# Kernel optimization log

Hardware: AMD Instinct MI355X
Metric: run time of the kernel (lower is better)

## Reference

```python
import jax, jax.numpy as jnp
import numpy as np

B, T, C = 4, 2048, 1024
H = 16
D = C // H  # head_dim = 64
SCALE = D ** -0.5


def setup_inputs() -> dict:
    key = jax.random.key(0)
    k1, k2, k3 = jax.random.split(key, 3)
    x = jax.random.normal(k1, (B, T, C), dtype=jnp.float32)
    w_qkv = jax.random.normal(k2, (C, 3 * C), dtype=jnp.float32) * (C ** -0.5)
    w_proj = jax.random.normal(k3, (C, C), dtype=jnp.float32) * (C ** -0.5)
    return {"x": x, "w_qkv": w_qkv, "w_proj": w_proj}


def reference(x, w_qkv, w_proj):
    Bx, Tx, Cx = x.shape
    qkv = x @ w_qkv                        # [B, T, 3C]
    q, k, v = jnp.split(qkv, 3, axis=-1)   # each [B, T, C]
    # [B, T, H, D] -> [B, H, T, D]
    q = q.reshape(Bx, Tx, H, D).transpose(0, 2, 1, 3)
    k = k.reshape(Bx, Tx, H, D).transpose(0, 2, 1, 3)
    v = v.reshape(Bx, Tx, H, D).transpose(0, 2, 1, 3)
    att = jnp.einsum('bhqd,bhkd->bhqk', q, k) * SCALE  # [B, H, T, T]
    causal = jnp.tril(jnp.ones((Tx, Tx), dtype=bool))
    att = jnp.where(causal[None, None], att, -jnp.inf)
    att = jax.nn.softmax(att, axis=-1)
    # dropout p=0.0 (eval-mode reference): identity
    y = jnp.einsum('bhqk,bhkd->bhqd', att, v)          # [B, H, T, D]
    y = y.transpose(0, 2, 1, 3).reshape(Bx, Tx, Cx)    # [B, T, C]
    return y @ w_proj
```

## Files before the change

kernel.cpp:

```cpp
#include <hip/hip_runtime.h>
#include <hip/hip_bf16.h>

#define Bdim 4
#define Tdim 2048
#define Cdim 1024
#define Hdim 16
#define Ddim 64
#define SCALE_Q 0.18033688011112042f

using f32x4  = __attribute__((ext_vector_type(4))) float;
using short8 = __attribute__((ext_vector_type(8))) short;

union U8 { uint4 v; unsigned short s[8]; };

__device__ __forceinline__ unsigned short f2bf(float f) {
  union { float f; unsigned int i; } x; x.f = f;
  unsigned int lsb = (x.i >> 16) & 1u;
  unsigned int r = x.i + 0x7fffu + lsb;
  return (unsigned short)(r >> 16);
}

__device__ __forceinline__ unsigned int pk_bf16(float lo, float hi) {
  union { __hip_bfloat162 h; unsigned int u; } c;
  c.h = __float22bfloat162_rn(make_float2(lo, hi));
  return c.u;
}

__device__ __forceinline__ float fexp2(float x) {
#if __has_builtin(__builtin_amdgcn_exp2f)
  return __builtin_amdgcn_exp2f(x);
#else
  return exp2f(x);
#endif
}

__device__ __forceinline__ void glds16(const unsigned short* g, unsigned short* l) {
  __builtin_amdgcn_global_load_lds(
      (const __attribute__((address_space(1))) void*)g,
      (__attribute__((address_space(3))) void*)l,
      16, 0, 0);
}

__device__ __forceinline__ int detect_fmt(const unsigned int* xw) {
  int cnt = 0;
  for (int i = 0; i < 64; i++) {
    unsigned int e = (xw[i] >> 7) & 0xFFu;
    if (e >= 100u && e <= 140u) cnt++;
  }
  return (cnt >= 40) ? 1 : 0;
}

__global__ void detect_kernel(const unsigned int* __restrict__ x, int* __restrict__ flag) {
  if (threadIdx.x == 0) *flag = detect_fmt(x);
}

__global__ __launch_bounds__(256) void prep_kernel(
    const void* __restrict__ x, const void* __restrict__ wq, const void* __restrict__ wp,
    unsigned short* __restrict__ X16, unsigned short* __restrict__ WqT,
    unsigned short* __restrict__ WpT, int* __restrict__ flag)
{
  __shared__ __align__(16) unsigned short Ts[64][72];
  __shared__ int sfmt;
  if (threadIdx.x == 0) {
    const int f = detect_fmt((const unsigned int*)x);
    sfmt = f;
    if (blockIdx.x == 0) *flag = f;
  }
  __syncthreads();
  const int fmt = sfmt;
  const unsigned bid = blockIdx.x;
  const int tid = threadIdx.x;

  if (bid < 4096u) {
    const size_t i = (size_t)bid * 256 + tid;
    if (fmt == 1) {
      *(uint4*)(X16 + i * 8) = *(const uint4*)((const unsigned short*)x + i * 8);
    } else {
      const float* s = (const float*)x + i * 8;
      float4 a = *(const float4*)(s);
      float4 b = *(const float4*)(s + 4);
      U8 o;
      o.s[0]=f2bf(a.x); o.s[1]=f2bf(a.y); o.s[2]=f2bf(a.z); o.s[3]=f2bf(a.w);
      o.s[4]=f2bf(b.x); o.s[5]=f2bf(b.y); o.s[6]=f2bf(b.z); o.s[7]=f2bf(b.w);
      *(uint4*)(X16 + i * 8) = o.v;
    }
    return;
  }

  const void* W; unsigned short* WT; int N, K, n0, k0;
  if (bid < 4864u) {
    const int t = bid - 4096;
    W = wq; WT = WqT; N = 3072; K = 1024;
    n0 = (t % 48) * 64; k0 = (t / 48) * 64;
  } else {
    const int t = bid - 4864;
    W = wp; WT = WpT; N = 1024; K = 1024;
    n0 = (t & 15) * 64; k0 = (t >> 4) * 64;
  }
  const int r = tid >> 2, c0 = (tid & 3) * 16;

  if (fmt == 0) {
    const float* Wf = (const float*)W + (size_t)(k0 + r) * N + n0 + c0;
    #pragma unroll
    for (int j4 = 0; j4 < 4; j4++) {
      float4 v = *(const float4*)(Wf + j4 * 4);
      Ts[r][c0 + j4*4 + 0] = f2bf(v.x);
      Ts[r][c0 + j4*4 + 1] = f2bf(v.y);
      Ts[r][c0 + j4*4 + 2] = f2bf(v.z);
      Ts[r][c0 + j4*4 + 3] = f2bf(v.w);
    }
  } else {
    const unsigned short* Wh = (const unsigned short*)W + (size_t)(k0 + r) * N + n0 + c0;
    uint4 v0 = *(const uint4*)(Wh);
    uint4 v1 = *(const uint4*)(Wh + 8);
    *(uint4*)&Ts[r][c0] = v0;
    *(uint4*)&Ts[r][c0 + 8] = v1;
  }
  __syncthreads();

  U8 o0, o1;
  #pragma unroll
  for (int j = 0; j < 8; j++) { o0.s[j] = Ts[c0 + j][r]; o1.s[j] = Ts[c0 + 8 + j][r]; }
  unsigned short* dst = WT + (size_t)(n0 + r) * K + k0 + c0;
  *(uint4*)(dst)     = o0.v;
  *(uint4*)(dst + 8) = o1.v;
}

__global__ __launch_bounds__(256) void gemm128d_kernel(
    const unsigned short* __restrict__ A16,
    const unsigned short* __restrict__ BT16,
    void* __restrict__ Cout,
    unsigned short* __restrict__ Qb,
    unsigned short* __restrict__ Kb,
    unsigned short* __restrict__ Vb,
    const int* __restrict__ flag,
    int M, int N, int K, int mode, int vT)
{
  __shared__ __align__(16) unsigned short As[2][128 * 32];
  __shared__ __align__(16) unsigned short Bs[2][128 * 32];

  const int fmt = *flag;
  const int tid  = threadIdx.x;
  const int wave = tid >> 6;
  const int lane = tid & 63;
  const int col  = lane & 15;
  const int quad = lane >> 4;
  const int m0 = blockIdx.x * 128;
  const int n0 = blockIdx.y * 128;
  const int wm = (wave >> 1) * 64;
  const int wn = (wave & 1) * 64;

  const int r4 = lane >> 2;
  const int schunk = ((lane & 3) ^ ((lane >> 3) & 3)) * 8;
  const int rsw = (quad ^ ((col >> 1) & 3)) * 8;

  f32x4 acc[4][4];
  #pragma unroll
  for (int i = 0; i < 4; i++)
    #pragma unroll
    for (int j = 0; j < 4; j++) acc[i][j] = (f32x4){0.f, 0.f, 0.f, 0.f};

  const unsigned short* ApA = A16  + (size_t)(m0 + wave * 32 + r4) * K + schunk;
  const unsigned short* ApB = ApA + (size_t)16 * K;
  const unsigned short* BpA = BT16 + (size_t)(n0 + wave * 32 + r4) * K + schunk;
  const unsigned short* BpB = BpA + (size_t)16 * K;

#define STAGE(BUF, KS) do { \
    glds16(ApA + (KS) * 32, &As[BUF][wave * 32 * 32]);        \
    glds16(ApB + (KS) * 32, &As[BUF][(wave * 32 + 16) * 32]); \
    glds16(BpA + (KS) * 32, &Bs[BUF][wave * 32 * 32]);        \
    glds16(BpB + (KS) * 32, &Bs[BUF][(wave * 32 + 16) * 32]); \
  } while (0)

#define COMPUTE(BUF) do { \
    short8 afr[4], bfr[4]; \
    _Pragma("unroll") \
    for (int mi = 0; mi < 4; mi++) \
      afr[mi] = *(const short8*)&As[BUF][(wm + mi * 16 + col) * 32 + rsw]; \
    _Pragma("unroll") \
    for (int ni = 0; ni < 4; ni++) \
      bfr[ni] = *(const short8*)&Bs[BUF][(wn + ni * 16 + col) * 32 + rsw]; \
    _Pragma("unroll") \
    for (int mi = 0; mi < 4; mi++) \
      _Pragma("unroll") \
      for (int ni = 0; ni < 4; ni++) \
        acc[mi][ni] = __builtin_amdgcn_mfma_f32_16x16x32_bf16(afr[mi], bfr[ni], acc[mi][ni], 0, 0, 0); \
  } while (0)

  const int NK = K >> 5;
  STAGE(0, 0);
  for (int ks = 0; ks < NK - 1; ++ks) {
    STAGE((ks + 1) & 1, ks + 1);
    asm volatile("s_waitcnt vmcnt(4)" ::: "memory");
    __builtin_amdgcn_s_barrier();
    __builtin_amdgcn_sched_barrier(0);
    COMPUTE(ks & 1);
    __builtin_amdgcn_sched_barrier(0);
    __builtin_amdgcn_s_barrier();
  }
  asm volatile("s_waitcnt vmcnt(0)" ::: "memory");
  __builtin_amdgcn_s_barrier();
  __builtin_amdgcn_sched_barrier(0);
  COMPUTE((NK - 1) & 1);
#undef STAGE
#undef COMPUTE

  if (mode == 1) {
    const int bb = m0 >> 11;
    const int tBase = (m0 & 2047) + wm;
    #pragma unroll
    for (int ni = 0; ni < 4; ni++) {
      const int n = n0 + wn + ni * 16 + col;
      const int which = n >> 10;
      const int rem = n & 1023;
      const int h = rem >> 6;
      const int d = rem & 63;
      if (which == 2 && vT) {
        unsigned short* base = Vb + (size_t)(bb * Hdim + h) * Tdim * Ddim
                                  + (size_t)d * Tdim + tBase;
        #pragma unroll
        for (int mi = 0; mi < 4; mi++) {
          const int t0 = mi * 16 + quad * 4;
          *(uint2*)(base + t0) = make_uint2(pk_bf16(acc[mi][ni][0], acc[mi][ni][1]),
                                            pk_bf16(acc[mi][ni][2], acc[mi][ni][3]));
        }
      } else {
        unsigned short* dstBase = (which == 0) ? Qb : (which == 1 ? Kb : Vb);
        const float scale = (which == 0) ? SCALE_Q : 1.f;
        dstBase += (size_t)(bb * Hdim + h) * Tdim * Ddim + d;
        #pragma unroll
        for (int mi = 0; mi < 4; mi++)
          #pragma unroll
          for (int i = 0; i < 4; i++) {
            const int t = tBase + mi * 16 + quad * 4 + i;
            dstBase[(size_t)t * Ddim] = f2bf(acc[mi][ni][i] * scale);
          }
      }
    }
  } else {
    #pragma unroll
    for (int mi = 0; mi < 4; mi++)
      #pragma unroll
      for (int ni = 0; ni < 4; ni++)
        #pragma unroll
        for (int i = 0; i < 4; i++) {
          const int m = m0 + wm + mi * 16 + quad * 4 + i;
          const int n = n0 + wn + ni * 16 + col;
          const float v = acc[mi][ni][i];
          if (fmt == 0) ((float*)Cout)[(size_t)m * N + n] = v;
          else ((unsigned short*)Cout)[(size_t)m * N + n] = f2bf(v);
        }
  }
}

#define BM 64
#define BN 64
#define BK 32
#define LDK 40

__global__ __launch_bounds__(256) void gemm64_kernel(
    const void* __restrict__ A,
    const void* __restrict__ Bw,
    void* __restrict__ Cout,
    unsigned short* __restrict__ Qb,
    unsigned short* __restrict__ Kb,
    unsigned short* __restrict__ Vb,
    const int* __restrict__ flag,
    int M, int N, int K, int mode, int aFmt, int outFmt, int aOff, int mOff)
{
  __shared__ __align__(16) unsigned short As[BM * LDK];
  __shared__ __align__(16) unsigned short Bs[BN * LDK];

  const int fmt = *flag;
  const int af  = (aFmt  == 2) ? fmt : aFmt;
  const int of  = (outFmt == 2) ? fmt : outFmt;

  const int tid  = threadIdx.x;
  const int wave = tid >> 6;
  const int lane = tid & 63;
  const int m0 = blockIdx.x * BM;
  const int n0 = blockIdx.y * BN;

  const int ar = tid >> 2;
  const int ak = (tid & 3) * 8;
  const int bk = tid >> 3;
  const int bn = (tid & 7) * 8;

  const int lr = lane & 15;
  const int lq = lane >> 4;

  f32x4 acc[4] = {{0,0,0,0},{0,0,0,0},{0,0,0,0},{0,0,0,0}};

  for (int k0 = 0; k0 < K; k0 += BK) {
    U8 a8;
    if (af == 1) {
      a8.v = *(const uint4*)((const unsigned short*)A + (size_t)(aOff + m0 + ar) * K + (k0 + ak));
    } else {
      const float* Af = (const float*)A + (size_t)(aOff + m0 + ar) * K + (k0 + ak);
      float4 x0 = *(const float4*)(Af);
      float4 x1 = *(const float4*)(Af + 4);
      a8.s[0] = f2bf(x0.x); a8.s[1] = f2bf(x0.y); a8.s[2] = f2bf(x0.z); a8.s[3] = f2bf(x0.w);
      a8.s[4] = f2bf(x1.x); a8.s[5] = f2bf(x1.y); a8.s[6] = f2bf(x1.z); a8.s[7] = f2bf(x1.w);
    }
    *(uint4*)(&As[ar * LDK + ak]) = a8.v;

    U8 b8;
    if (fmt == 1) {
      b8.v = *(const uint4*)((const unsigned short*)Bw + (size_t)(k0 + bk) * N + (n0 + bn));
    } else {
      const float* Bf = (const float*)Bw + (size_t)(k0 + bk) * N + (n0 + bn);
      float4 x0 = *(const float4*)(Bf);
      float4 x1 = *(const float4*)(Bf + 4);
      b8.s[0] = f2bf(x0.x); b8.s[1] = f2bf(x0.y); b8.s[2] = f2bf(x0.z); b8.s[3] = f2bf(x0.w);
      b8.s[4] = f2bf(x1.x); b8.s[5] = f2bf(x1.y); b8.s[6] = f2bf(x1.z); b8.s[7] = f2bf(x1.w);
    }
    #pragma unroll
    for (int i = 0; i < 8; i++) Bs[(bn + i) * LDK + bk] = b8.s[i];
    __syncthreads();

    short8 afrag = *(const short8*)(&As[(wave * 16 + lr) * LDK + lq * 8]);
    #pragma unroll
    for (int c = 0; c < 4; c++) {
      short8 bfrag = *(const short8*)(&Bs[(c * 16 + lr) * LDK + lq * 8]);
      acc[c] = __builtin_amdgcn_mfma_f32_16x16x32_bf16(afrag, bfrag, acc[c], 0, 0, 0);
    }
    __syncthreads();
  }

  #pragma unroll
  for (int c = 0; c < 4; c++) {
    #pragma unroll
    for (int i = 0; i < 4; i++) {
      const int m = m0 + wave * 16 + lq * 4 + i;
      const int n = n0 + c * 16 + lr;
      const float v = acc[c][i];
      if (mode == 0) {
        if (of == 0) ((float*)Cout)[(size_t)(mOff + m) * N + n] = v;
        else ((unsigned short*)Cout)[(size_t)(mOff + m) * N + n] = f2bf(v);
      } else {
        const int which = n >> 10;
        const int rem = n & 1023;
        const int h = rem >> 6;
        const int d = rem & 63;
        const int b = m >> 11;
        const int t = m & 2047;
        const size_t idx = ((size_t)(b * Hdim + h) * Tdim + t) * Ddim + d;
        if      (which == 0) Qb[idx] = f2bf(v * SCALE_Q);
        else if (which == 1) Kb[idx] = f2bf(v);
        else                 Vb[idx] = f2bf(v);
      }
    }
  }
}

__global__ __launch_bounds__(256) void attn128_kernel(
    const unsigned short* __restrict__ Qb,
    const unsigned short* __restrict__ Kb,
    const unsigned short* __restrict__ VbT,
    unsigned short* __restrict__ Y)
{
  __shared__ __align__(16) unsigned short Ks[2][64 * 64];
  __shared__ __align__(16) unsigned short Vt[2][64 * 64];
  __shared__ __align__(16) unsigned short Pw[4][32 * 64];

  const int tid  = threadIdx.x;
  const int wave = tid >> 6;
  const int lane = tid & 63;
  const int col  = lane & 15;
  const int quad = lane >> 4;
  const int cx   = col & 7;
  const int ch0  = (quad ^ cx) * 8;
  const int ch1  = ch0 ^ 32;

  const int srow = lane >> 3;
  const int sx   = ((lane & 7) ^ (srow & 7)) * 8;

  const int pair = blockIdx.x >> 6;
  const int bh   = blockIdx.x & 63;
  const size_t headOff = (size_t)bh * Tdim * Ddim;
  const int b = bh >> 4;
  const int h = bh & 15;

  const short8 onesf = {16256, 16256, 16256, 16256, 16256, 16256, 16256, 16256};

#define ASTAGE(BUF, KB) do { \
    const unsigned short* Ksrc = Kb + headOff + (size_t)((KB) + wave * 16 + srow) * Ddim + sx; \
    glds16(Ksrc,            &Ks[BUF][(wave * 16) * 64]);      \
    glds16(Ksrc + 8 * Ddim, &Ks[BUF][(wave * 16 + 8) * 64]);  \
    const unsigned short* Vsrc = VbT + headOff + (size_t)(wave * 16 + srow) * Tdim + (KB) + sx; \
    glds16(Vsrc,            &Vt[BUF][(wave * 16) * 64]);      \
    glds16(Vsrc + 8 * Tdim, &Vt[BUF][(wave * 16 + 8) * 64]);  \
  } while (0)

  #pragma unroll
  for (int half = 0; half < 2; half++) {
    const int qt = half ? (15 - pair) : pair;
    const int qb = qt * 128;
    const int nkt = (qb >> 6) + 2;
    const int rMin = qb + wave * 32;
    const int rMax = rMin + 31;

    short8 qf[2][2];
    #pragma unroll
    for (int mi = 0; mi < 2; mi++) {
      const unsigned short* Qr = Qb + headOff + (size_t)(rMin + mi * 16 + col) * Ddim;
      qf[mi][0] = *(const short8*)(Qr + quad * 8);
      qf[mi][1] = *(const short8*)(Qr + 32 + quad * 8);
    }

    f32x4 o_acc[2][4];
    f32x4 l_acc[2];
    #pragma unroll
    for (int mi = 0; mi < 2; mi++) {
      l_acc[mi] = (f32x4){0.f, 0.f, 0.f, 0.f};
      #pragma unroll
      for (int n = 0; n < 4; n++) o_acc[mi][n] = (f32x4){0.f, 0.f, 0.f, 0.f};
    }

    ASTAGE(0, 0);
    for (int kt = 0; kt < nkt; kt++) {
      const int cur = kt & 1;
      if (kt + 1 < nkt) {
        ASTAGE(cur ^ 1, (kt + 1) * 64);
        asm volatile("s_waitcnt vmcnt(4)" ::: "memory");
      } else {
        asm volatile("s_waitcnt vmcnt(0)" ::: "memory");
      }
      __builtin_amdgcn_s_barrier();
      __builtin_amdgcn_sched_barrier(0);

      const int ktb = kt * 64;
      if (ktb <= rMax) {
        f32x4 s_acc[4][2];
        #pragma unroll
        for (int c = 0; c < 4; c++) {
          const unsigned short* Kl = &Ks[cur][(c * 16 + col) * 64];
          short8 kf0 = *(const short8*)(Kl + ch0);
          short8 kf1 = *(const short8*)(Kl + ch1);
          #pragma unroll
          for (int mi = 0; mi < 2; mi++) {
            f32x4 z = {0.f, 0.f, 0.f, 0.f};
            z = __builtin_amdgcn_mfma_f32_16x16x32_bf16(kf0, qf[mi][0], z, 0, 0, 0);
            s_acc[c][mi] = __builtin_amdgcn_mfma_f32_16x16x32_bf16(kf1, qf[mi][1], z, 0, 0, 0);
          }
        }

        if (ktb + 63 > rMin) {
          #pragma unroll
          for (int c = 0; c < 4; c++)
            #pragma unroll
            for (int mi = 0; mi < 2; mi++)
              #pragma unroll
              for (int i = 0; i < 4; i++)
                if (ktb + c * 16 + quad * 4 + i > rMin + mi * 16 + col)
                  s_acc[c][mi][i] = -1e30f;
        }

        #pragma unroll
        for (int mi = 0; mi < 2; mi++)
          #pragma unroll
          for (int c = 0; c < 4; c++) {
            const float p0 = fexp2(s_acc[c][mi][0]);
            const float p1 = fexp2(s_acc[c][mi][1]);
            const float p2 = fexp2(s_acc[c][mi][2]);
            const float p3 = fexp2(s_acc[c][mi][3]);
            const unsigned int u0 = pk_bf16(p0, p1);
            const unsigned int u1 = pk_bf16(p2, p3);
            const int po = (((c * 2 + (quad >> 1)) ^ cx) * 8) + (quad & 1) * 4;
            *(uint2*)&Pw[wave][(mi * 16 + col) * 64 + po] = make_uint2(u0, u1);
          }

        short8 pf[2][2];
        #pragma unroll
        for (int mi = 0; mi < 2; mi++) {
          pf[mi][0] = *(const short8*)(&Pw[wave][(mi * 16 + col) * 64 + ch0]);
          pf[mi][1] = *(const short8*)(&Pw[wave][(mi * 16 + col) * 64 + ch1]);
          l_acc[mi] = __builtin_amdgcn_mfma_f32_16x16x32_bf16(pf[mi][0], onesf, l_acc[mi], 0, 0, 0);
          l_acc[mi] = __builtin_amdgcn_mfma_f32_16x16x32_bf16(pf[mi][1], onesf, l_acc[mi], 0, 0, 0);
        }
        #pragma unroll
        for (int n = 0; n < 4; n++) {
          const unsigned short* Vl = &Vt[cur][(n * 16 + col) * 64];
          short8 vf0 = *(const short8*)(Vl + ch0);
          short8 vf1 = *(const short8*)(Vl + ch1);
          #pragma unroll
          for (int mi = 0; mi < 2; mi++) {
            o_acc[mi][n] = __builtin_amdgcn_mfma_f32_16x16x32_bf16(pf[mi][0], vf0, o_acc[mi][n], 0, 0, 0);
            o_acc[mi][n] = __builtin_amdgcn_mfma_f32_16x16x32_bf16(pf[mi][1], vf1, o_acc[mi][n], 0, 0, 0);
          }
        }
      }
      __builtin_amdgcn_sched_barrier(0);
      __builtin_amdgcn_s_barrier();
    }

    #pragma unroll
    for (int mi = 0; mi < 2; mi++)
      #pragma unroll
      for (int i = 0; i < 4; i++) {
        const float inv = 1.f / l_acc[mi][i];
        const int qrow = rMin + mi * 16 + quad * 4 + i;
        unsigned short* dst = Y + (size_t)(b * Tdim + qrow) * Cdim + h * Ddim;
        #pragma unroll
        for (int n = 0; n < 4; n++)
          dst[n * 16 + col] = f2bf(o_acc[mi][n][i] * inv);
      }
  }
#undef ASTAGE
}

__global__ __launch_bounds__(256) void attn128_legacy_kernel(
    const unsigned short* __restrict__ Qb,
    const unsigned short* __restrict__ Kb,
    const unsigned short* __restrict__ Vb,
    const unsigned short* __restrict__ VbT,
    unsigned short* __restrict__ Y)
{
  __shared__ __align__(16) unsigned short Ks[64 * 72];
  __shared__ __align__(16) unsigned short Vt[64 * 72];
  __shared__ __align__(16) unsigned short Pw[4][32 * 72];

  const int tid  = threadIdx.x;
  const int wave = tid >> 6;
  const int lane = tid & 63;
  const int col  = lane & 15;
  const int quad = lane >> 4;

  const int pair = blockIdx.x & 7;
  const int bh   = blockIdx.x >> 3;
  const size_t headOff = (size_t)bh * Tdim * Ddim;

  const int sr = tid >> 2;
  const int sc = (tid & 3) * 16;

  const int b = bh >> 4;
  const int h = bh & 15;

  const short8 onesf = {16256, 16256, 16256, 16256, 16256, 16256, 16256, 16256};

  #pragma unroll
  for (int half = 0; half < 2; half++) {
    const int qt = half ? (15 - pair) : pair;
    const int qb = qt * 128;
    const int nkt = (qb >> 6) + 2;
    const int rMin = qb + wave * 32;
    const int rMax = rMin + 31;

    short8 qf[2][2];
    #pragma unroll
    for (int mi = 0; mi < 2; mi++) {
      const unsigned short* Qr = Qb + headOff + (size_t)(rMin + mi * 16 + col) * Ddim;
      qf[mi][0] = *(const short8*)(Qr + quad * 8);
      qf[mi][1] = *(const short8*)(Qr + 32 + quad * 8);
    }

    f32x4 o_acc[2][4];
    f32x4 l_acc[2];
    #pragma unroll
    for (int mi = 0; mi < 2; mi++) {
      l_acc[mi] = (f32x4){0.f, 0.f, 0.f, 0.f};
      #pragma unroll
      for (int n = 0; n < 4; n++) o_acc[mi][n] = (f32x4){0.f, 0.f, 0.f, 0.f};
    }

    uint4 kr0, kr1, vr0, vr1;
    {
      const unsigned short* Kr = Kb + headOff + (size_t)sr * Ddim + sc;
      kr0 = *(const uint4*)(Kr);
      kr1 = *(const uint4*)(Kr + 8);
      if (VbT) {
        const unsigned short* Vr = VbT + headOff + (size_t)sr * Tdim + sc;
        vr0 = *(const uint4*)(Vr);
        vr1 = *(const uint4*)(Vr + 8);
      } else {
        const unsigned short* Vr = Vb + headOff + (size_t)sr * Ddim + sc;
        vr0 = *(const uint4*)(Vr);
        vr1 = *(const uint4*)(Vr + 8);
      }
    }

    for (int kt = 0; kt < nkt; kt++) {
      __syncthreads();
      *(uint4*)&Ks[sr * 72 + sc]     = kr0;
      *(uint4*)&Ks[sr * 72 + sc + 8] = kr1;
      if (VbT) {
        *(uint4*)&Vt[sr * 72 + sc]     = vr0;
        *(uint4*)&Vt[sr * 72 + sc + 8] = vr1;
      } else {
        U8 v0, v1; v0.v = vr0; v1.v = vr1;
        #pragma unroll
        for (int j = 0; j < 8; j++) {
          Vt[(sc + j) * 72 + sr]     = v0.s[j];
          Vt[(sc + 8 + j) * 72 + sr] = v1.s[j];
        }
      }
      __syncthreads();

      if (kt + 1 < nkt) {
        const int kb = (kt + 1) * 64;
        const unsigned short* Kr = Kb + headOff + (size_t)(kb + sr) * Ddim + sc;
        kr0 = *(const uint4*)(Kr);
        kr1 = *(const uint4*)(Kr + 8);
        if (VbT) {
          const unsigned short* Vr = VbT + headOff + (size_t)sr * Tdim + kb + sc;
          vr0 = *(const uint4*)(Vr);
          vr1 = *(const uint4*)(Vr + 8);
        } else {
          const unsigned short* Vr = Vb + headOff + (size_t)(kb + sr) * Ddim + sc;
          vr0 = *(const uint4*)(Vr);
          vr1 = *(const uint4*)(Vr + 8);
        }
      }

      const int ktb = kt * 64;
      if (ktb <= rMax) {
        f32x4 s_acc[4][2];
        #pragma unroll
        for (int c = 0; c < 4; c++) {
          const unsigned short* Kl = &Ks[(c * 16 + col) * 72];
          short8 kf0 = *(const short8*)(Kl + quad * 8);
          short8 kf1 = *(const short8*)(Kl + 32 + quad * 8);
          #pragma unroll
          for (int mi = 0; mi < 2; mi++) {
            f32x4 z = {0.f, 0.f, 0.f, 0.f};
            z = __builtin_amdgcn_mfma_f32_16x16x32_bf16(kf0, qf[mi][0], z, 0, 0, 0);
            s_acc[c][mi] = __builtin_amdgcn_mfma_f32_16x16x32_bf16(kf1, qf[mi][1], z, 0, 0, 0);
          }
        }

        if (ktb + 63 > rMin) {
          #pragma unroll
          for (int c = 0; c < 4; c++)
            #pragma unroll
            for (int mi = 0; mi < 2; mi++)
              #pragma unroll
              for (int i = 0; i < 4; i++)
                if (ktb + c * 16 + quad * 4 + i > rMin + mi * 16 + col)
                  s_acc[c][mi][i] = -1e30f;
        }

        #pragma unroll
        for (int mi = 0; mi < 2; mi++)
          #pragma unroll
          for (int c = 0; c < 4; c++) {
            const float p0 = fexp2(fminf(s_acc[c][mi][0], 80.f));
            const float p1 = fexp2(fminf(s_acc[c][mi][1], 80.f));
            const float p2 = fexp2(fminf(s_acc[c][mi][2], 80.f));
            const float p3 = fexp2(fminf(s_acc[c][mi][3], 80.f));
            const unsigned int u0 = pk_bf16(p0, p1);
            const unsigned int u1 = pk_bf16(p2, p3);
            uint2* dst = (uint2*)&Pw[wave][(mi * 16 + col) * 72 + c * 16 + quad * 4];
            *dst = make_uint2(u0, u1);
          }

        short8 pf[2][2];
        #pragma unroll
        for (int mi = 0; mi < 2; mi++) {
          pf[mi][0] = *(const short8*)(&Pw[wave][(mi * 16 + col) * 72 + quad * 8]);
          pf[mi][1] = *(const short8*)(&Pw[wave][(mi * 16 + col) * 72 + 32 + quad * 8]);
          l_acc[mi] = __builtin_amdgcn_mfma_f32_16x16x32_bf16(pf[mi][0], onesf, l_acc[mi], 0, 0, 0);
          l_acc[mi] = __builtin_amdgcn_mfma_f32_16x16x32_bf16(pf[mi][1], onesf, l_acc[mi], 0, 0, 0);
        }
        #pragma unroll
        for (int n = 0; n < 4; n++) {
          const unsigned short* Vl = &Vt[(n * 16 + col) * 72];
          short8 vf0 = *(const short8*)(Vl + quad * 8);
          short8 vf1 = *(const short8*)(Vl + 32 + quad * 8);
          #pragma unroll
          for (int mi = 0; mi < 2; mi++) {
            o_acc[mi][n] = __builtin_amdgcn_mfma_f32_16x16x32_bf16(pf[mi][0], vf0, o_acc[mi][n], 0, 0, 0);
            o_acc[mi][n] = __builtin_amdgcn_mfma_f32_16x16x32_bf16(pf[mi][1], vf1, o_acc[mi][n], 0, 0, 0);
          }
        }
      }
    }

    #pragma unroll
    for (int mi = 0; mi < 2; mi++)
      #pragma unroll
      for (int i = 0; i < 4; i++) {
        const float inv = 1.f / l_acc[mi][i];
        const int qrow = rMin + mi * 16 + quad * 4 + i;
        unsigned short* dst = Y + (size_t)(b * Tdim + qrow) * Cdim + h * Ddim;
        #pragma unroll
        for (int n = 0; n < 4; n++)
          dst[n * 16 + col] = f2bf(o_acc[mi][n][i] * inv);
      }
  }
}

extern "C" void kernel_launch(void* const* d_in, const int* in_sizes, int n_in,
                              void* d_out, int out_size, void* d_ws, size_t ws_size,
                              hipStream_t stream) {
  const void* x      = d_in[0];
  const void* w_qkv  = d_in[1];
  const void* w_proj = d_in[2];

  int* flag = (int*)d_ws;
  unsigned short* wsb = (unsigned short*)((char*)d_ws + 1024);

  const size_t HS = (size_t)Bdim * Hdim * Tdim * Ddim;
  const size_t FULL  = 1024 + 2 * (4 * HS + (size_t)3072 * 1024 + (size_t)1024 * 1024);
  const size_t FULL2 = FULL + 2 * HS;
  const size_t MONO  = 1024 + 2 * (4 * HS);

  dim3 blk(256);

  if (ws_size >= FULL) {
    unsigned short* Qb  = wsb;
    unsigned short* Kb  = Qb + HS;
    unsigned short* Vb  = Kb + HS;
    unsigned short* XY  = Vb + HS;
    unsigned short* WqT = XY + HS;
    unsigned short* WpT = WqT + (size_t)3072 * 1024;
    unsigned short* VbT = WpT + (size_t)1024 * 1024;
    const int M = Bdim * Tdim;

    prep_kernel<<<dim3(5120), blk, 0, stream>>>(x, w_qkv, w_proj, XY, WqT, WpT, flag);

    if (ws_size >= FULL2) {
      gemm128d_kernel<<<dim3(M / 128, 3072 / 128), blk, 0, stream>>>(
          XY, WqT, nullptr, Qb, Kb, VbT, flag, M, 3072, Cdim, 1, 1);
      attn128_kernel<<<dim3(Bdim * Hdim * 8), blk, 0, stream>>>(Qb, Kb, VbT, XY);
    } else {
      gemm128d_kernel<<<dim3(M / 128, 3072 / 128), blk, 0, stream>>>(
          XY, WqT, nullptr, Qb, Kb, Vb, flag, M, 3072, Cdim, 1, 0);
      attn128_legacy_kernel<<<dim3(Bdim * Hdim * 8), blk, 0, stream>>>(Qb, Kb, Vb, nullptr, XY);
    }

    gemm128d_kernel<<<dim3(M / 128, Cdim / 128), blk, 0, stream>>>(
        XY, WpT, d_out, nullptr, nullptr, nullptr, flag, M, Cdim, Cdim, 0, 0);
  } else if (ws_size >= MONO) {
    detect_kernel<<<1, 64, 0, stream>>>((const unsigned int*)x, flag);
    const size_t HSb = (size_t)Hdim * Tdim * Ddim;
    unsigned short* Qb2 = wsb;
    unsigned short* Kb2 = Qb2 + HSb;
    unsigned short* Vb2 = Kb2 + HSb;
    unsigned short* Y2  = Vb2 + HSb;
    for (int b = 0; b < Bdim; b++) {
      gemm64_kernel<<<dim3(Tdim / BM, 3072 / BN), blk, 0, stream>>>(
          x, w_qkv, nullptr, Qb2, Kb2, Vb2, flag,
          Tdim, 3072, Cdim, 1, 2, 2, b * Tdim, 0);
      attn128_legacy_kernel<<<dim3(Hdim * 8), blk, 0, stream>>>(Qb2, Kb2, Vb2, nullptr, Y2);
      gemm64_kernel<<<dim3(Tdim / BM, Cdim / BN), blk, 0, stream>>>(
          Y2, w_proj, d_out, nullptr, nullptr, nullptr, flag,
          Tdim, Cdim, Cdim, 0, 1, 2, 0, b * Tdim);
    }
  } else {
    detect_kernel<<<1, 64, 0, stream>>>((const unsigned int*)x, flag);
    const size_t HSb = (size_t)Hdim * Tdim * Ddim;
    unsigned short* Qb = wsb;
    unsigned short* Kb = Qb + HSb;
    unsigned short* Vb = Kb + HSb;
    unsigned short* Y2 = Vb + HSb;

    for (int b = 0; b < Bdim; b++) {
      gemm64_kernel<<<dim3(Tdim / BM, 3072 / BN), blk, 0, stream>>>(
          x, w_qkv, nullptr, Qb, Kb, Vb, flag,
          Tdim, 3072, Cdim, 1, 2, 2, b * Tdim, 0);

      attn128_legacy_kernel<<<dim3(Hdim * 8), blk, 0, stream>>>(Qb, Kb, Vb, nullptr, Y2);

      gemm64_kernel<<<dim3(Tdim / BM, Cdim / BN), blk, 0, stream>>>(
          Y2, w_proj, d_out, nullptr, nullptr, nullptr, flag,
          Tdim, Cdim, Cdim, 0, 1, 2, 0, b * Tdim);
    }
  }
}
```

Measured before the change: 250.0 us.

## Shrink attention query tile to 64 rows and double grid size

Attention now uses 64-row query tiles, with each wave owning 16 rows instead of 32, and pairs tile qt with 31-qt for causal load balance. The grid grows from 512 to 1024 blocks, and the per-tile diagonal skip logic is simplified so only the last key tile is masked. This raises occupancy and parallelism across the GPU's compute units, but halves the reuse of each staged K/V tile across query rows. That roughly doubles K/V global traffic per query and the number of barriers per unit of work.

Result: faster. 244.2 us (-2.3%).

```diff
diff --git a/kernel.cpp b/kernel.cpp
--- a/kernel.cpp
+++ b/kernel.cpp
@@ -353,7 +353,7 @@
   }
 }
 
-__global__ __launch_bounds__(256) void attn128_kernel(
+__global__ __launch_bounds__(256) void attn64_kernel(
     const unsigned short* __restrict__ Qb,
     const unsigned short* __restrict__ Kb,
     const unsigned short* __restrict__ VbT,
@@ -361,7 +361,7 @@
 {
   __shared__ __align__(16) unsigned short Ks[2][64 * 64];
   __shared__ __align__(16) unsigned short Vt[2][64 * 64];
-  __shared__ __align__(16) unsigned short Pw[4][32 * 64];
+  __shared__ __align__(16) unsigned short Pw[4][16 * 64];
 
   const int tid  = threadIdx.x;
   const int wave = tid >> 6;
@@ -394,28 +394,22 @@
 
   #pragma unroll
   for (int half = 0; half < 2; half++) {
-    const int qt = half ? (15 - pair) : pair;
-    const int qb = qt * 128;
-    const int nkt = (qb >> 6) + 2;
-    const int rMin = qb + wave * 32;
-    const int rMax = rMin + 31;
-
-    short8 qf[2][2];
-    #pragma unroll
-    for (int mi = 0; mi < 2; mi++) {
-      const unsigned short* Qr = Qb + headOff + (size_t)(rMin + mi * 16 + col) * Ddim;
-      qf[mi][0] = *(const short8*)(Qr + quad * 8);
-      qf[mi][1] = *(const short8*)(Qr + 32 + quad * 8);
-    }
-
-    f32x4 o_acc[2][4];
-    f32x4 l_acc[2];
-    #pragma unroll
-    for (int mi = 0; mi < 2; mi++) {
-      l_acc[mi] = (f32x4){0.f, 0.f, 0.f, 0.f};
-      #pragma unroll
-      for (int n = 0; n < 4; n++) o_acc[mi][n] = (f32x4){0.f, 0.f, 0.f, 0.f};
-    }
+    const int qt = half ? (31 - pair) : pair;
+    const int qb = qt * 64;
+    const int nkt = qt + 1;
+    const int rMin = qb + wave * 16;
+
+    short8 qf[2];
+    {
+      const unsigned short* Qr = Qb + headOff + (size_t)(rMin + col) * Ddim;
+      qf[0] = *(const short8*)(Qr + quad * 8);
+      qf[1] = *(const short8*)(Qr + 32 + quad * 8);
+    }
+
+    f32x4 o_acc[4];
+    f32x4 l_acc = (f32x4){0.f, 0.f, 0.f, 0.f};
+    #pragma unroll
+    for (int n = 0; n < 4; n++) o_acc[n] = (f32x4){0.f, 0.f, 0.f, 0.f};
 
     ASTAGE(0, 0);
     for (int kt = 0; kt < nkt; kt++) {
@@ -429,82 +423,64 @@
       __builtin_amdgcn_s_barrier();
       __builtin_amdgcn_sched_barrier(0);
 
-      const int ktb = kt * 64;
-      if (ktb <= rMax) {
-        f32x4 s_acc[4][2];
-        #pragma unroll
-        for (int c = 0; c < 4; c++) {
-          const unsigned short* Kl = &Ks[cur][(c * 16 + col) * 64];
-          short8 kf0 = *(const short8*)(Kl + ch0);
-          short8 kf1 = *(const short8*)(Kl + ch1);
+      f32x4 s_acc[4];
+      #pragma unroll
+      for (int c = 0; c < 4; c++) {
+        const unsigned short* Kl = &Ks[cur][(c * 16 + col) * 64];
+        short8 kf0 = *(const short8*)(Kl + ch0);
+        short8 kf1 = *(const short8*)(Kl + ch1);
+        f32x4 z = {0.f, 0.f, 0.f, 0.f};
+        z = __builtin_amdgcn_mfma_f32_16x16x32_bf16(kf0, qf[0], z, 0, 0, 0);
+        s_acc[c] = __builtin_amdgcn_mfma_f32_16x16x32_bf16(kf1, qf[1], z, 0, 0, 0);
+      }
+
+      if (kt == nkt - 1) {
+        #pragma unroll
+        for (int c = 0; c < 4; c++)
           #pragma unroll
-          for (int mi = 0; mi < 2; mi++) {
-            f32x4 z = {0.f, 0.f, 0.f, 0.f};
-            z = __builtin_amdgcn_mfma_f32_16x16x32_bf16(kf0, qf[mi][0], z, 0, 0, 0);
-            s_acc[c][mi] = __builtin_amdgcn_mfma_f32_16x16x32_bf16(kf1, qf[mi][1], z, 0, 0, 0);
-          }
-        }
-
-        if (ktb + 63 > rMin) {
-          #pragma unroll
-          for (int c = 0; c < 4; c++)
-            #pragma unroll
-            for (int mi = 0; mi < 2; mi++)
-              #pragma unroll
-              for (int i = 0; i < 4; i++)
-                if (ktb + c * 16 + quad * 4 + i > rMin + mi * 16 + col)
-                  s_acc[c][mi][i] = -1e30f;
-        }
-
-        #pragma unroll
-        for (int mi = 0; mi < 2; mi++)
-          #pragma unroll
-          for (int c = 0; c < 4; c++) {
-            const float p0 = fexp2(s_acc[c][mi][0]);
-            const float p1 = fexp2(s_acc[c][mi][1]);
-            const float p2 = fexp2(s_acc[c][mi][2]);
-            const float p3 = fexp2(s_acc[c][mi][3]);
-            const unsigned int u0 = pk_bf16(p0, p1);
-            const unsigned int u1 = pk_bf16(p2, p3);
-            const int po = (((c * 2 + (quad >> 1)) ^ cx) * 8) + (quad & 1) * 4;
-            *(uint2*)&Pw[wave][(mi * 16 + col) * 64 + po] = make_uint2(u0, u1);
-          }
-
-        short8 pf[2][2];
-        #pragma unroll
-        for (int mi = 0; mi < 2; mi++) {
-          pf[mi][0] = *(const short8*)(&Pw[wave][(mi * 16 + col) * 64 + ch0]);
-          pf[mi][1] = *(const short8*)(&Pw[wave][(mi * 16 + col) * 64 + ch1]);
-          l_acc[mi] = __builtin_amdgcn_mfma_f32_16x16x32_bf16(pf[mi][0], onesf, l_acc[mi], 0, 0, 0);
-          l_acc[mi] = __builtin_amdgcn_mfma_f32_16x16x32_bf16(pf[mi][1], onesf, l_acc[mi], 0, 0, 0);
-        }
-        #pragma unroll
-        for (int n = 0; n < 4; n++) {
-          const unsigned short* Vl = &Vt[cur][(n * 16 + col) * 64];
-          short8 vf0 = *(const short8*)(Vl + ch0);
-          short8 vf1 = *(const short8*)(Vl + ch1);
-          #pragma unroll
-          for (int mi = 0; mi < 2; mi++) {
-            o_acc[mi][n] = __builtin_amdgcn_mfma_f32_16x16x32_bf16(pf[mi][0], vf0, o_acc[mi][n], 0, 0, 0);
-            o_acc[mi][n] = __builtin_amdgcn_mfma_f32_16x16x32_bf16(pf[mi][1], vf1, o_acc[mi][n], 0, 0, 0);
-          }
-        }
-      }
+          for (int i = 0; i < 4; i++)
+            if (qb + c * 16 + quad * 4 + i > rMin + col)
+              s_acc[c][i] = -1e30f;
+      }
+
+      #pragma unroll
+      for (int c = 0; c < 4; c++) {
+        const float p0 = fexp2(s_acc[c][0]);
+        const float p1 = fexp2(s_acc[c][1]);
+        const float p2 = fexp2(s_acc[c][2]);
+        const float p3 = fexp2(s_acc[c][3]);
+        const unsigned int u0 = pk_bf16(p0, p1);
+        const unsigned int u1 = pk_bf16(p2, p3);
+        const int po = (((c * 2 + (quad >> 1)) ^ cx) * 8) + (quad & 1) * 4;
+        *(uint2*)&Pw[wave][col * 64 + po] = make_uint2(u0, u1);
+      }
+
+      short8 pf0 = *(const short8*)(&Pw[wave][col * 64 + ch0]);
+      short8 pf1 = *(const short8*)(&Pw[wave][col * 64 + ch1]);
+      l_acc = __builtin_amdgcn_mfma_f32_16x16x32_bf16(pf0, onesf, l_acc, 0, 0, 0);
+      l_acc = __builtin_amdgcn_mfma_f32_16x16x32_bf16(pf1, onesf, l_acc, 0, 0, 0);
+      #pragma unroll
+      for (int n = 0; n < 4; n++) {
+        const unsigned short* Vl = &Vt[cur][(n * 16 + col) * 64];
+        short8 vf0 = *(const short8*)(Vl + ch0);
+        short8 vf1 = *(const short8*)(Vl + ch1);
+        o_acc[n] = __builtin_amdgcn_mfma_f32_16x16x32_bf16(pf0, vf0, o_acc[n], 0, 0, 0);
+        o_acc[n] = __builtin_amdgcn_mfma_f32_16x16x32_bf16(pf1, vf1, o_acc[n], 0, 0, 0);
+      }
+
       __builtin_amdgcn_sched_barrier(0);
       __builtin_amdgcn_s_barrier();
     }
 
     #pragma unroll
-    for (int mi = 0; mi < 2; mi++)
+    for (int i = 0; i < 4; i++) {
+      const float inv = 1.f / l_acc[i];
+      const int qrow = rMin + quad * 4 + i;
+      unsigned short* dst = Y + (size_t)(b * Tdim + qrow) * Cdim + h * Ddim;
       #pragma unroll
-      for (int i = 0; i < 4; i++) {
-        const float inv = 1.f / l_acc[mi][i];
-        const int qrow = rMin + mi * 16 + quad * 4 + i;
-        unsigned short* dst = Y + (size_t)(b * Tdim + qrow) * Cdim + h * Ddim;
-        #pragma unroll
-        for (int n = 0; n < 4; n++)
-          dst[n * 16 + col] = f2bf(o_acc[mi][n][i] * inv);
-      }
+      for (int n = 0; n < 4; n++)
+        dst[n * 16 + col] = f2bf(o_acc[n][i] * inv);
+    }
   }
 #undef ASTAGE
 }
@@ -721,7 +697,7 @@
     if (ws_size >= FULL2) {
       gemm128d_kernel<<<dim3(M / 128, 3072 / 128), blk, 0, stream>>>(
           XY, WqT, nullptr, Qb, Kb, VbT, flag, M, 3072, Cdim, 1, 1);
-      attn128_kernel<<<dim3(Bdim * Hdim * 8), blk, 0, stream>>>(Qb, Kb, VbT, XY);
+      attn64_kernel<<<dim3(16 * 64), blk, 0, stream>>>(Qb, Kb, VbT, XY);
     } else {
       gemm128d_kernel<<<dim3(M / 128, 3072 / 128), blk, 0, stream>>>(
           XY, WqT, nullptr, Qb, Kb, Vb, flag, M, 3072, Cdim, 1, 0);
```
